# Performance work log

Hardware: AMD Instinct MI355X
Metric: run time of the kernel (lower is better)

Reference implementation:

```python
import jax, jax.numpy as jnp
import numpy as np

B, N, DIM = 4, 2048, 128
K = 32            # num_nearest_neighbors
FF = 4            # fourier_features
M_DIM = 16
EDGE_IN = FF * 2 + DIM * 2 + 1  # 265


def setup_inputs() -> dict:
    key = jax.random.key(0)
    ks = jax.random.split(key, 16)
    std = 0.001  # init_eps normal init for Linear weights
    p = {
        "feats": jax.random.normal(ks[0], (B, N, DIM), jnp.float32),
        "coors": jax.random.normal(ks[1], (B, N, 3), jnp.float32),
        # edge_mlp: Linear(265, 530) -> SiLU -> Linear(530, 16) -> SiLU
        "eW1": jax.random.normal(ks[2], (EDGE_IN, EDGE_IN * 2), jnp.float32) * std,
        "eb1": jax.random.normal(ks[3], (EDGE_IN * 2,), jnp.float32) * std,
        "eW2": jax.random.normal(ks[4], (EDGE_IN * 2, M_DIM), jnp.float32) * std,
        "eb2": jax.random.normal(ks[5], (M_DIM,), jnp.float32) * std,
        # coors_mlp: Linear(16, 64) -> SiLU -> Linear(64, 1)
        "cW1": jax.random.normal(ks[6], (M_DIM, M_DIM * 4), jnp.float32) * std,
        "cb1": jax.random.normal(ks[7], (M_DIM * 4,), jnp.float32) * std,
        "cW2": jax.random.normal(ks[8], (M_DIM * 4, 1), jnp.float32) * std,
        "cb2": jax.random.normal(ks[9], (1,), jnp.float32) * std,
        # node_mlp: Linear(144, 256) -> SiLU -> Linear(256, 128)
        "nW1": jax.random.normal(ks[10], (DIM + M_DIM, DIM * 2), jnp.float32) * std,
        "nb1": jax.random.normal(ks[11], (DIM * 2,), jnp.float32) * std,
        "nW2": jax.random.normal(ks[12], (DIM * 2, DIM), jnp.float32) * std,
        "nb2": jax.random.normal(ks[13], (DIM,), jnp.float32) * std,
    }
    return p


def _egnn_fwd(feats, coors, eW1, eb1, eW2, eb2, cW1, cb1, cW2, cb2, nW1, nb1, nW2, nb2):
    # all-pairs squared distances: [b, n, n]
    rel_coors_full = coors[:, :, None, :] - coors[:, None, :, :]
    rel_dist = jnp.sum(rel_coors_full * rel_coors_full, axis=-1)

    # top-k nearest (smallest distance) -> indices [b, n, k]
    _, idx = jax.lax.top_k(-rel_dist, K)

    # gather neighbor coords / feats per batch: [b, n, k, *]
    coors_j = jax.vmap(lambda x, i: x[i])(coors, idx)
    feats_j = jax.vmap(lambda x, i: x[i])(feats, idx)
    rel_coors = coors[:, :, None, :] - coors_j                     # b n k 3
    d = jnp.take_along_axis(rel_dist, idx, axis=2)[..., None]       # b n k 1

    # fourier encode distances: [b, n, k, 2*FF + 1]
    scales = 2.0 ** jnp.arange(FF, dtype=feats.dtype)               # [FF]
    xs = d[..., None] / scales                                      # b n k 1 FF
    enc = jnp.concatenate([jnp.sin(xs), jnp.cos(xs), d[..., None]], axis=-1)
    enc = enc[..., 0, :]                                            # b n k (2FF+1)

    feats_i = jnp.broadcast_to(feats[:, :, None, :], feats_j.shape)
    edge_input = jnp.concatenate([feats_i, feats_j, enc], axis=-1)  # b n k 265

    # edge MLP -> messages m_ij [b, n, k, m_dim]
    h = jax.nn.silu(edge_input @ eW1 + eb1)
    m_ij = jax.nn.silu(h @ eW2 + eb2)

    # coors MLP -> per-edge coordinate weights [b, n, k]
    cw = (jax.nn.silu(m_ij @ cW1 + cb1) @ cW2 + cb2)[..., 0]
    coors_out = jnp.einsum('bij,bijc->bic', cw, rel_coors) + coors

    # node update: sum-pool messages, concat with feats, MLP + residual
    m_i = jnp.sum(m_ij, axis=-2)                                    # b n m_dim
    node_in = jnp.concatenate([feats, m_i], axis=-1)
    node_out = jax.nn.silu(node_in @ nW1 + nb1) @ nW2 + nb2 + feats
    return node_out, coors_out


def reference(feats, coors, eW1, eb1, eW2, eb2, cW1, cb1, cW2, cb2, nW1, nb1, nW2, nb2):
    return _egnn_fwd(feats, coors, eW1, eb1, eW2, eb2, cW1, cb1, cW2, cb2, nW1, nb1, nW2, nb2)
```

## Files before the change

### kernel.cpp

```cpp
#include <hip/hip_runtime.h>
#include <hip/hip_bf16.h>
#include <math.h>

#define Bb 4
#define Nn 2048
#define DIMd 128
#define Kk 32
#define H1 530
#define PW2 530
#define MD 16
#define NDH 256
#define NDI 144
#define TOPK_BLKS (Bb*Nn/4)
#define PMAT_BLKS (Bb*Nn/32)

typedef float f32x2 __attribute__((ext_vector_type(2)));
typedef float f32x4 __attribute__((ext_vector_type(4)));
typedef short s16x8 __attribute__((ext_vector_type(8)));

__device__ __forceinline__ unsigned short f2bf(float f){
    union { float f; unsigned u; } v; v.f = f;
    unsigned r = v.u + 0x7FFFu + ((v.u >> 16) & 1u);
    return (unsigned short)(r >> 16);
}
__device__ __forceinline__ float silu_f(float x){
    float e = __builtin_amdgcn_exp2f(x * -1.442695041f);
    return x * __builtin_amdgcn_rcpf(1.0f + e);
}
__device__ __forceinline__ f32x2 silu2(f32x2 x){
    float e0 = __builtin_amdgcn_exp2f(x[0] * -1.442695041f);
    float e1 = __builtin_amdgcn_exp2f(x[1] * -1.442695041f);
    f32x2 r;
    r[0] = x[0] * __builtin_amdgcn_rcpf(1.0f + e0);
    r[1] = x[1] * __builtin_amdgcn_rcpf(1.0f + e1);
    return r;
}
__device__ __forceinline__ unsigned cvt_pk_bf16(float a, float b){
    unsigned r;
    asm("v_cvt_pk_bf16_f32 %0, %1, %2" : "=v"(r) : "v"(a), "v"(b));
    return r;
}

__global__ __launch_bounds__(256) void fragw_kernel(const float* __restrict__ eW1,
        const float* __restrict__ eW2,
        unsigned short* __restrict__ W1F, unsigned short* __restrict__ WPF,
        unsigned short* __restrict__ W2F2){
    int i0 = blockIdx.x * 256 + threadIdx.x;
    int stride = gridDim.x * 256;
    for (int i = i0; i < 34*5*512; i += stride){
        int j = i & 7, lane = (i >> 3) & 63, t = i >> 9;
        int ks = t % 5, nt = t / 5;
        int cg = nt*16 + (lane & 15);
        int k = ks*32 + ((lane >> 4) << 3) + j;
        float v = 0.f;
        if (cg < H1){
            if (k < 128) v = eW1[(size_t)(128+k)*H1 + cg];
            else if (k < 137) v = eW1[(size_t)(256+(k-128))*H1 + cg];
        }
        W1F[i] = f2bf(v);
    }
    for (int i = i0; i < 34*4*512; i += stride){
        int j = i & 7, lane = (i >> 3) & 63, t = i >> 9;
        int ks = t & 3, nt = t >> 2;
        int cg = nt*16 + (lane & 15);
        int k = ks*32 + ((lane >> 4) << 3) + j;
        float v = (cg < H1) ? eW1[(size_t)k*H1 + cg] : 0.f;
        WPF[i] = f2bf(v);
    }
    for (int i = i0; i < 34*512; i += stride){
        int j = i & 7, lane = (i >> 3) & 63, nt = i >> 9;
        int kl = ((lane >> 4) << 3) + j;
        int col = lane & 15;
        int row = nt*16 + kl;
        float v = (kl < 16 && row < H1) ? eW2[(size_t)row*MD + col] : 0.f;
        W2F2[i] = f2bf(v);
    }
}

__global__ __launch_bounds__(256) void prep_kernel(const float* __restrict__ coors,
        const float* __restrict__ feats,
        const unsigned short* __restrict__ WPF, const float* __restrict__ eb1,
        int* __restrict__ idx_ws, float* __restrict__ dv_ws, float* __restrict__ P){
    int bid = blockIdx.x;
    int tid = threadIdx.x;
    if (bid < TOPK_BLKS){
        int w = tid >> 6, lane = tid & 63;
        int node = bid * 4 + w;
        int b = node >> 11;
        const float* cbp = coors + (size_t)b * Nn * 3;
        float cx = coors[node*3+0], cy = coors[node*3+1], cz = coors[node*3+2];
        float d[32];
        #pragma unroll
        for (int t = 0; t < 32; t++){
            int j = t*64 + lane;
            float dx = cx - cbp[j*3+0], dy = cy - cbp[j*3+1], dz = cz - cbp[j*3+2];
            d[t] = dx*dx + dy*dy + dz*dz;
        }
        float md = d[0]; int mj = lane;
        #pragma unroll
        for (int t = 1; t < 32; t++){
            int jt = t*64 + lane;
            if (d[t] < md){ md = d[t]; mj = jt; }
        }
        for (int r = 0; r < Kk; r++){
            float bd = md; int bj = mj;
            #pragma unroll
            for (int off = 32; off; off >>= 1){
                float d2 = __shfl_xor(bd, off); int j2 = __shfl_xor(bj, off);
                if (d2 < bd || (d2 == bd && j2 < bj)){ bd = d2; bj = j2; }
            }
            if (lane == 0){
                idx_ws[node*Kk + r] = bj;
                dv_ws[node*Kk + r] = bd;
            }
            if (mj == bj){
                md = 3.4e38f; mj = 0x7fffffff;
                #pragma unroll
                for (int t = 0; t < 32; t++){
                    int jt = t*64 + lane;
                    if (jt == bj) d[t] = 3.4e38f;
                    if (d[t] < md){ md = d[t]; mj = jt; }
                }
            }
        }
    } else {
        int wid = tid >> 6, lane = tid & 63;
        int node0 = (bid - TOPK_BLKS) * 32;
        int kg = (lane >> 4) * 8;
        s16x8 af[2][4];
        #pragma unroll
        for (int m = 0; m < 2; m++){
            const float* fr = feats + (size_t)(node0 + m*16 + (lane & 15)) * DIMd;
            #pragma unroll
            for (int ks = 0; ks < 4; ks++){
                f32x4 lo = *(const f32x4*)(fr + ks*32 + kg);
                f32x4 hi = *(const f32x4*)(fr + ks*32 + kg + 4);
                union { s16x8 v; unsigned u[4]; } pk;
                pk.u[0] = cvt_pk_bf16(lo[0], lo[1]); pk.u[1] = cvt_pk_bf16(lo[2], lo[3]);
                pk.u[2] = cvt_pk_bf16(hi[0], hi[1]); pk.u[3] = cvt_pk_bf16(hi[2], hi[3]);
                af[m][ks] = pk.v;
            }
        }
        const s16x8* WPFv = (const s16x8*)WPF;
        for (int nt = wid; nt < 34; nt += 4){
            f32x4 acc0 = {0,0,0,0}, acc1 = {0,0,0,0};
            #pragma unroll
            for (int ks = 0; ks < 4; ks++){
                s16x8 bb = WPFv[(nt*4 + ks)*64 + lane];
                acc0 = __builtin_amdgcn_mfma_f32_16x16x32_bf16(af[0][ks], bb, acc0, 0, 0, 0);
                acc1 = __builtin_amdgcn_mfma_f32_16x16x32_bf16(af[1][ks], bb, acc1, 0, 0, 0);
            }
            int cg = nt*16 + (lane & 15);
            if (cg < H1){
                float b = eb1[cg];
                int r0 = (lane >> 4) * 4;
                #pragma unroll
                for (int r = 0; r < 4; r++){
                    P[(size_t)(node0 + r0 + r)*PW2 + cg]      = acc0[r] + b;
                    P[(size_t)(node0 + 16 + r0 + r)*PW2 + cg] = acc1[r] + b;
                }
            }
        }
    }
}

__global__ __launch_bounds__(256, 4) void edge_kernel(const float* __restrict__ coors,
        const float* __restrict__ feats, const float* __restrict__ eb2,
        const float* __restrict__ cW1, const float* __restrict__ cb1,
        const float* __restrict__ cW2, const float* __restrict__ cb2,
        const float* __restrict__ P, const unsigned short* __restrict__ W1F,
        const unsigned short* __restrict__ W2F2,
        const int* __restrict__ idx_ws, const float* __restrict__ dv_ws,
        float* __restrict__ mi_ws, float* __restrict__ coors_out){
    __shared__ float Pi_lds[544];
    __shared__ __align__(16) unsigned short aenc[Kk][32];
    __shared__ int js[Kk];
    __shared__ float rels[Kk][3];
    __shared__ float m_red[4][Kk][MD+1];
    __shared__ float cacc[4][3];

    int node = blockIdx.x; int tid = threadIdx.x;
    int b = node >> 11;
    int wid = tid >> 6, lane = tid & 63;

    const float* Pn = P + (size_t)node*PW2;
    Pi_lds[tid]       = Pn[tid];
    { int c = tid + 256; Pi_lds[c] = (c < PW2) ? Pn[c] : 0.f; }
    if (tid < 32){ int c = 512 + tid; Pi_lds[c] = (c < PW2) ? Pn[c] : 0.f; }
    if (tid < Kk){
        int j = idx_ws[node*Kk + tid];
        float dv = dv_ws[node*Kk + tid];
        js[tid] = j;
        unsigned short e[9];
        e[0] = f2bf(sinf(dv));        e[1] = f2bf(sinf(dv*0.5f));
        e[2] = f2bf(sinf(dv*0.25f));  e[3] = f2bf(sinf(dv*0.125f));
        e[4] = f2bf(cosf(dv));        e[5] = f2bf(cosf(dv*0.5f));
        e[6] = f2bf(cosf(dv*0.25f));  e[7] = f2bf(cosf(dv*0.125f));
        e[8] = f2bf(dv);
        #pragma unroll
        for (int q = 0; q < 9; q++) aenc[tid][q] = e[q];
        #pragma unroll
        for (int q = 9; q < 32; q++) aenc[tid][q] = 0;
        int jg = (b << 11) + j;
        rels[tid][0] = coors[node*3+0] - coors[jg*3+0];
        rels[tid][1] = coors[node*3+1] - coors[jg*3+1];
        rels[tid][2] = coors[node*3+2] - coors[jg*3+2];
    }
    __syncthreads();

    int kg = (lane >> 4) * 8;
    int grp = lane >> 4, n16 = lane & 15;
    s16x8 af[2][5];
    #pragma unroll
    for (int m = 0; m < 2; m++){
        int row = m*16 + n16;
        int jgl = (b << 11) + js[row];
        const float* fr = feats + (size_t)jgl * DIMd;
        #pragma unroll
        for (int ks = 0; ks < 4; ks++){
            f32x4 lo = *(const f32x4*)(fr + ks*32 + kg);
            f32x4 hi = *(const f32x4*)(fr + ks*32 + kg + 4);
            union { s16x8 v; unsigned u[4]; } pk;
            pk.u[0] = cvt_pk_bf16(lo[0], lo[1]); pk.u[1] = cvt_pk_bf16(lo[2], lo[3]);
            pk.u[2] = cvt_pk_bf16(hi[0], hi[1]); pk.u[3] = cvt_pk_bf16(hi[2], hi[3]);
            af[m][ks] = pk.v;
        }
        af[m][4] = *(const s16x8*)(&aenc[row][kg]);
    }

    int addr1 = ((((2*grp)    ) << 4) | n16) << 2;
    int addr2 = ((((2*grp) + 1) << 4) | n16) << 2;

    const s16x8* W1Fv  = (const s16x8*)W1F;
    const s16x8* W2F2v = (const s16x8*)W2F2;
    f32x4 macc0 = {0,0,0,0}, macc1 = {0,0,0,0};
    for (int nt = wid; nt < 34; nt += 4){
        f32x4 acc0 = {0,0,0,0}, acc1 = {0,0,0,0};
        #pragma unroll
        for (int ks = 0; ks < 5; ks++){
            s16x8 aw = W1Fv[(nt*5 + ks)*64 + lane];
            acc0 = __builtin_amdgcn_mfma_f32_16x16x32_bf16(aw, af[0][ks], acc0, 0, 0, 0);
            acc1 = __builtin_amdgcn_mfma_f32_16x16x32_bf16(aw, af[1][ks], acc1, 0, 0, 0);
        }
        s16x8 w2a = W2F2v[nt*64 + lane];
        int cgb = nt*16 + grp*4;
        float x0[4], x1[4];
        #pragma unroll
        for (int r = 0; r < 4; r++){
            int cg = cgb + r;
            bool valid = cg < H1;
            float pic = Pi_lds[cg];
            x0[r] = valid ? silu_f(acc0[r] + pic) : 0.f;
            x1[r] = valid ? silu_f(acc1[r] + pic) : 0.f;
        }
        unsigned p00 = cvt_pk_bf16(x0[0], x0[1]), p01 = cvt_pk_bf16(x0[2], x0[3]);
        unsigned p10 = cvt_pk_bf16(x1[0], x1[1]), p11 = cvt_pk_bf16(x1[2], x1[3]);
        union { s16x8 v; int u[4]; } b0, b1;
        b0.u[0] = __builtin_amdgcn_ds_bpermute(addr1, (int)p00);
        b0.u[1] = __builtin_amdgcn_ds_bpermute(addr1, (int)p01);
        b0.u[2] = __builtin_amdgcn_ds_bpermute(addr2, (int)p00);
        b0.u[3] = __builtin_amdgcn_ds_bpermute(addr2, (int)p01);
        b1.u[0] = __builtin_amdgcn_ds_bpermute(addr1, (int)p10);
        b1.u[1] = __builtin_amdgcn_ds_bpermute(addr1, (int)p11);
        b1.u[2] = __builtin_amdgcn_ds_bpermute(addr2, (int)p10);
        b1.u[3] = __builtin_amdgcn_ds_bpermute(addr2, (int)p11);
        macc0 = __builtin_amdgcn_mfma_f32_16x16x32_bf16(w2a, b0.v, macc0, 0, 0, 0);
        macc1 = __builtin_amdgcn_mfma_f32_16x16x32_bf16(w2a, b1.v, macc1, 0, 0, 0);
    }
    #pragma unroll
    for (int r = 0; r < 4; r++){
        m_red[wid][n16][grp*4 + r]      = macc0[r];
        m_red[wid][16 + n16][grp*4 + r] = macc1[r];
    }
    __syncthreads();
    #pragma unroll
    for (int t = tid; t < Kk*MD; t += 256){
        int n = t >> 4, f = t & 15;
        float s = m_red[0][n][f] + m_red[1][n][f] + m_red[2][n][f] + m_red[3][n][f];
        m_red[0][n][f] = silu_f(s + eb2[f]);
    }
    __syncthreads();
    if (tid < MD){
        float s = 0.f;
        #pragma unroll
        for (int n = 0; n < Kk; n++) s += m_red[0][n][tid];
        mi_ws[node*MD + tid] = s;
    }
    float vx = 0.f, vy = 0.f, vz = 0.f;
    int u4 = n16 * 4;
    f32x4 cb14 = *(const f32x4*)(cb1 + u4);
    f32x4 c24  = *(const f32x4*)(cW2 + u4);
    #pragma unroll
    for (int q = 0; q < 2; q++){
        int eid = wid*8 + grp*2 + q;
        f32x4 acc4 = cb14;
        #pragma unroll
        for (int f = 0; f < MD; f++){
            float mv = m_red[0][eid][f];
            f32x4 w4 = *(const f32x4*)(cW1 + f*64 + u4);
            acc4 += (f32x4){mv,mv,mv,mv} * w4;
        }
        float p = silu_f(acc4[0])*c24[0] + silu_f(acc4[1])*c24[1]
                + silu_f(acc4[2])*c24[2] + silu_f(acc4[3])*c24[3];
        #pragma unroll
        for (int off = 1; off < 16; off <<= 1) p += __shfl_xor(p, off);
        float cw = p + cb2[0];
        if (n16 == 0){
            vx += cw * rels[eid][0];
            vy += cw * rels[eid][1];
            vz += cw * rels[eid][2];
        }
    }
    vx += __shfl_xor(vx, 16); vx += __shfl_xor(vx, 32);
    vy += __shfl_xor(vy, 16); vy += __shfl_xor(vy, 32);
    vz += __shfl_xor(vz, 16); vz += __shfl_xor(vz, 32);
    if (lane == 0){ cacc[wid][0] = vx; cacc[wid][1] = vy; cacc[wid][2] = vz; }
    __syncthreads();
    if (tid == 0){
        coors_out[node*3+0] = cacc[0][0]+cacc[1][0]+cacc[2][0]+cacc[3][0] + coors[node*3+0];
        coors_out[node*3+1] = cacc[0][1]+cacc[1][1]+cacc[2][1]+cacc[3][1] + coors[node*3+1];
        coors_out[node*3+2] = cacc[0][2]+cacc[1][2]+cacc[2][2]+cacc[3][2] + coors[node*3+2];
    }
}

__global__ __launch_bounds__(256) void node_kernel(const float* __restrict__ feats,
        const float* __restrict__ mi_ws,
        const float* __restrict__ nW1, const float* __restrict__ nb1,
        const float* __restrict__ nW2, const float* __restrict__ nb2,
        float* __restrict__ out){
    __shared__ float insT[NDI][12];
    __shared__ float hsdT[NDH][12];
    int tid = threadIdx.x;
    int node0 = blockIdx.x * 8;
    for (int t = tid; t < 8*DIMd; t += 256){
        int m = t >> 7, k = t & 127;
        insT[k][m] = feats[(size_t)node0*DIMd + t];
    }
    if (tid < 8*MD) insT[DIMd + (tid & 15)][tid >> 4] = mi_ws[node0*MD + tid];
    __syncthreads();
    float bias = nb1[tid];
    f32x2 acc[4];
    #pragma unroll
    for (int p = 0; p < 4; p++) acc[p] = (f32x2){bias, bias};
    for (int k = 0; k < NDI; k++){
        float wv = nW1[(size_t)k*NDH + tid];
        f32x2 w2 = {wv, wv};
        acc[0] += *(const f32x2*)&insT[k][0] * w2;
        acc[1] += *(const f32x2*)&insT[k][2] * w2;
        acc[2] += *(const f32x2*)&insT[k][4] * w2;
        acc[3] += *(const f32x2*)&insT[k][6] * w2;
    }
    #pragma unroll
    for (int p = 0; p < 4; p++) *(f32x2*)&hsdT[tid][2*p] = silu2(acc[p]);
    __syncthreads();
    int c = tid & 127, half = tid >> 7;
    float b2 = nb2[c];
    f32x2 a0 = {b2, b2}, a1 = {b2, b2};
    for (int k = 0; k < NDH; k++){
        float wv = nW2[(size_t)k*DIMd + c];
        f32x2 w2 = {wv, wv};
        a0 += *(const f32x2*)&hsdT[k][half*4]     * w2;
        a1 += *(const f32x2*)&hsdT[k][half*4 + 2] * w2;
    }
    #pragma unroll
    for (int q = 0; q < 4; q++){
        int m = half*4 + q;
        float v = (q < 2) ? a0[q & 1] : a1[q & 1];
        out[(size_t)(node0+m)*DIMd + c] = v + feats[(size_t)(node0+m)*DIMd + c];
    }
}

extern "C" void kernel_launch(void* const* d_in, const int* in_sizes, int n_in,
                              void* d_out, int out_size, void* d_ws, size_t ws_size,
                              hipStream_t stream){
    const float* feats = (const float*)d_in[0];
    const float* coors = (const float*)d_in[1];
    const float* eW1 = (const float*)d_in[2];
    const float* eb1 = (const float*)d_in[3];
    const float* eW2 = (const float*)d_in[4];
    const float* eb2 = (const float*)d_in[5];
    const float* cW1 = (const float*)d_in[6];
    const float* cb1 = (const float*)d_in[7];
    const float* cW2 = (const float*)d_in[8];
    const float* cb2 = (const float*)d_in[9];
    const float* nW1 = (const float*)d_in[10];
    const float* nb1 = (const float*)d_in[11];
    const float* nW2 = (const float*)d_in[12];
    const float* nb2 = (const float*)d_in[13];
    float* out = (float*)d_out;
    float* coors_out = out + (size_t)Bb*Nn*DIMd;

    char* ws = (char*)d_ws;
    size_t off = 0;
    int*   idx_ws = (int*)(ws + off);   off += (1u<<20);
    float* dv_ws  = (float*)(ws + off); off += (1u<<20);
    float* Pd     = (float*)(ws + off); off += 17367040u;
    float* mi_ws  = (float*)(ws + off); off += 524288u;
    unsigned short* W1F  = (unsigned short*)(ws + off); off += 174080u;
    unsigned short* WPF  = (unsigned short*)(ws + off); off += 139264u;
    unsigned short* W2F2 = (unsigned short*)(ws + off); off += 34816u;

    fragw_kernel<<<256, 256, 0, stream>>>(eW1, eW2, W1F, WPF, W2F2);
    prep_kernel<<<TOPK_BLKS + PMAT_BLKS, 256, 0, stream>>>(coors, feats, WPF, eb1,
                                                           idx_ws, dv_ws, Pd);
    edge_kernel<<<Bb*Nn, 256, 0, stream>>>(coors, feats, eb2, cW1, cb1, cW2, cb2,
                                           Pd, W1F, W2F2, idx_ws, dv_ws, mi_ws, coors_out);
    node_kernel<<<Bb*Nn/8, 256, 0, stream>>>(feats, mi_ws, nW1, nb1, nW2, nb2, out);
}
```

Before: 321.1 us.

## Move coords MLP and message pooling from edge kernel into node kernel

The edge kernel now stops after producing per-edge messages and writes the full m_ij tensor to a new workspace. A new finish_kernel does the coors MLP per edge (one thread per edge), the message sum-pool and the node MLP, all in one place. This shrinks the edge kernel's register and LDS footprint so the launch bound can go from 4 to 6 waves, and it drops the bounds check in the SiLU loop. The cost is an extra 16 MB of global writes and reads for m_ij, and the padded columns now rely on zero weights and padded Pi_lds.

```diff
diff --git a/kernel.cpp b/kernel.cpp
--- a/kernel.cpp
+++ b/kernel.cpp
@@ -164,20 +164,16 @@
     }
 }
 
-__global__ __launch_bounds__(256, 4) void edge_kernel(const float* __restrict__ coors,
+__global__ __launch_bounds__(256, 6) void edge_kernel(
         const float* __restrict__ feats, const float* __restrict__ eb2,
-        const float* __restrict__ cW1, const float* __restrict__ cb1,
-        const float* __restrict__ cW2, const float* __restrict__ cb2,
         const float* __restrict__ P, const unsigned short* __restrict__ W1F,
         const unsigned short* __restrict__ W2F2,
         const int* __restrict__ idx_ws, const float* __restrict__ dv_ws,
-        float* __restrict__ mi_ws, float* __restrict__ coors_out){
+        float* __restrict__ m_ws){
     __shared__ float Pi_lds[544];
     __shared__ __align__(16) unsigned short aenc[Kk][32];
     __shared__ int js[Kk];
-    __shared__ float rels[Kk][3];
     __shared__ float m_red[4][Kk][MD+1];
-    __shared__ float cacc[4][3];
 
     int node = blockIdx.x; int tid = threadIdx.x;
     int b = node >> 11;
@@ -201,10 +197,6 @@
         for (int q = 0; q < 9; q++) aenc[tid][q] = e[q];
         #pragma unroll
         for (int q = 9; q < 32; q++) aenc[tid][q] = 0;
-        int jg = (b << 11) + j;
-        rels[tid][0] = coors[node*3+0] - coors[jg*3+0];
-        rels[tid][1] = coors[node*3+1] - coors[jg*3+1];
-        rels[tid][2] = coors[node*3+2] - coors[jg*3+2];
     }
     __syncthreads();
 
@@ -247,11 +239,9 @@
         float x0[4], x1[4];
         #pragma unroll
         for (int r = 0; r < 4; r++){
-            int cg = cgb + r;
-            bool valid = cg < H1;
-            float pic = Pi_lds[cg];
-            x0[r] = valid ? silu_f(acc0[r] + pic) : 0.f;
-            x1[r] = valid ? silu_f(acc1[r] + pic) : 0.f;
+            float pic = Pi_lds[cgb + r];
+            x0[r] = silu_f(acc0[r] + pic);
+            x1[r] = silu_f(acc1[r] + pic);
         }
         unsigned p00 = cvt_pk_bf16(x0[0], x0[1]), p01 = cvt_pk_bf16(x0[2], x0[3]);
         unsigned p10 = cvt_pk_bf16(x1[0], x1[1]), p11 = cvt_pk_bf16(x1[2], x1[3]);
@@ -277,71 +267,76 @@
     for (int t = tid; t < Kk*MD; t += 256){
         int n = t >> 4, f = t & 15;
         float s = m_red[0][n][f] + m_red[1][n][f] + m_red[2][n][f] + m_red[3][n][f];
-        m_red[0][n][f] = silu_f(s + eb2[f]);
-    }
-    __syncthreads();
-    if (tid < MD){
-        float s = 0.f;
-        #pragma unroll
-        for (int n = 0; n < Kk; n++) s += m_red[0][n][tid];
-        mi_ws[node*MD + tid] = s;
-    }
-    float vx = 0.f, vy = 0.f, vz = 0.f;
-    int u4 = n16 * 4;
-    f32x4 cb14 = *(const f32x4*)(cb1 + u4);
-    f32x4 c24  = *(const f32x4*)(cW2 + u4);
-    #pragma unroll
-    for (int q = 0; q < 2; q++){
-        int eid = wid*8 + grp*2 + q;
-        f32x4 acc4 = cb14;
-        #pragma unroll
-        for (int f = 0; f < MD; f++){
-            float mv = m_red[0][eid][f];
-            f32x4 w4 = *(const f32x4*)(cW1 + f*64 + u4);
-            acc4 += (f32x4){mv,mv,mv,mv} * w4;
-        }
-        float p = silu_f(acc4[0])*c24[0] + silu_f(acc4[1])*c24[1]
-                + silu_f(acc4[2])*c24[2] + silu_f(acc4[3])*c24[3];
-        #pragma unroll
-        for (int off = 1; off < 16; off <<= 1) p += __shfl_xor(p, off);
-        float cw = p + cb2[0];
-        if (n16 == 0){
-            vx += cw * rels[eid][0];
-            vy += cw * rels[eid][1];
-            vz += cw * rels[eid][2];
-        }
-    }
-    vx += __shfl_xor(vx, 16); vx += __shfl_xor(vx, 32);
-    vy += __shfl_xor(vy, 16); vy += __shfl_xor(vy, 32);
-    vz += __shfl_xor(vz, 16); vz += __shfl_xor(vz, 32);
-    if (lane == 0){ cacc[wid][0] = vx; cacc[wid][1] = vy; cacc[wid][2] = vz; }
-    __syncthreads();
-    if (tid == 0){
-        coors_out[node*3+0] = cacc[0][0]+cacc[1][0]+cacc[2][0]+cacc[3][0] + coors[node*3+0];
-        coors_out[node*3+1] = cacc[0][1]+cacc[1][1]+cacc[2][1]+cacc[3][1] + coors[node*3+1];
-        coors_out[node*3+2] = cacc[0][2]+cacc[1][2]+cacc[2][2]+cacc[3][2] + coors[node*3+2];
-    }
-}
-
-__global__ __launch_bounds__(256) void node_kernel(const float* __restrict__ feats,
-        const float* __restrict__ mi_ws,
+        m_ws[(size_t)node*(Kk*MD) + t] = silu_f(s + eb2[f]);
+    }
+}
+
+__global__ __launch_bounds__(256) void finish_kernel(const float* __restrict__ feats,
+        const float* __restrict__ coors,
+        const float* __restrict__ m_ws, const int* __restrict__ idx_ws,
+        const float* __restrict__ cW1, const float* __restrict__ cb1,
+        const float* __restrict__ cW2, const float* __restrict__ cb2,
         const float* __restrict__ nW1, const float* __restrict__ nb1,
         const float* __restrict__ nW2, const float* __restrict__ nb2,
-        float* __restrict__ out){
+        float* __restrict__ out, float* __restrict__ coors_out){
+    __shared__ float msh[8][Kk][MD+1];
     __shared__ float insT[NDI][12];
     __shared__ float hsdT[NDH][12];
     int tid = threadIdx.x;
     int node0 = blockIdx.x * 8;
-    for (int t = tid; t < 8*DIMd; t += 256){
-        int m = t >> 7, k = t & 127;
-        insT[k][m] = feats[(size_t)node0*DIMd + t];
-    }
-    if (tid < 8*MD) insT[DIMd + (tid & 15)][tid >> 4] = mi_ws[node0*MD + tid];
+    const float* mp = m_ws + (size_t)node0*(Kk*MD);
+    for (int t = tid; t < 8*Kk*MD; t += 256)
+        msh[t >> 9][(t >> 4) & 31][t & 15] = mp[t];
+    for (int t = tid; t < 8*DIMd; t += 256)
+        insT[t & 127][t >> 7] = feats[(size_t)node0*DIMd + t];
+    int nl = tid >> 5, n = tid & 31;
+    int node = node0 + nl;
+    int b = node >> 11;
+    int j = idx_ws[node*Kk + n];
+    int jg = (b << 11) + j;
+    float rx = coors[node*3+0] - coors[jg*3+0];
+    float ry = coors[node*3+1] - coors[jg*3+1];
+    float rz = coors[node*3+2] - coors[jg*3+2];
+    __syncthreads();
+    if (tid < 128){
+        int m = tid >> 4, f = tid & 15;
+        float s = 0.f;
+        #pragma unroll
+        for (int q = 0; q < Kk; q++) s += msh[m][q][f];
+        insT[DIMd + f][m] = s;
+    }
+    float mv[MD];
+    #pragma unroll
+    for (int f = 0; f < MD; f++) mv[f] = msh[nl][n][f];
+    float p = 0.f;
+    #pragma unroll 4
+    for (int ug = 0; ug < 16; ug++){
+        f32x4 a4 = *(const f32x4*)(cb1 + ug*4);
+        #pragma unroll
+        for (int f = 0; f < MD; f++){
+            f32x4 w4 = *(const f32x4*)(cW1 + f*64 + ug*4);
+            a4 += (f32x4){mv[f],mv[f],mv[f],mv[f]} * w4;
+        }
+        f32x4 c4 = *(const f32x4*)(cW2 + ug*4);
+        p += silu_f(a4[0])*c4[0] + silu_f(a4[1])*c4[1]
+           + silu_f(a4[2])*c4[2] + silu_f(a4[3])*c4[3];
+    }
+    float cw = p + cb2[0];
+    float vx = cw*rx, vy = cw*ry, vz = cw*rz;
+    #pragma unroll
+    for (int off = 1; off < 32; off <<= 1){
+        vx += __shfl_xor(vx, off); vy += __shfl_xor(vy, off); vz += __shfl_xor(vz, off);
+    }
+    if (n == 0){
+        coors_out[node*3+0] = vx + coors[node*3+0];
+        coors_out[node*3+1] = vy + coors[node*3+1];
+        coors_out[node*3+2] = vz + coors[node*3+2];
+    }
     __syncthreads();
     float bias = nb1[tid];
     f32x2 acc[4];
     #pragma unroll
-    for (int p = 0; p < 4; p++) acc[p] = (f32x2){bias, bias};
+    for (int q = 0; q < 4; q++) acc[q] = (f32x2){bias, bias};
     for (int k = 0; k < NDI; k++){
         float wv = nW1[(size_t)k*NDH + tid];
         f32x2 w2 = {wv, wv};
@@ -351,7 +346,7 @@
         acc[3] += *(const f32x2*)&insT[k][6] * w2;
     }
     #pragma unroll
-    for (int p = 0; p < 4; p++) *(f32x2*)&hsdT[tid][2*p] = silu2(acc[p]);
+    for (int q = 0; q < 4; q++) *(f32x2*)&hsdT[tid][2*q] = silu2(acc[q]);
     __syncthreads();
     int c = tid & 127, half = tid >> 7;
     float b2 = nb2[c];
@@ -395,7 +390,7 @@
     int*   idx_ws = (int*)(ws + off);   off += (1u<<20);
     float* dv_ws  = (float*)(ws + off); off += (1u<<20);
     float* Pd     = (float*)(ws + off); off += 17367040u;
-    float* mi_ws  = (float*)(ws + off); off += 524288u;
+    float* m_ws   = (float*)(ws + off); off += 16777216u;
     unsigned short* W1F  = (unsigned short*)(ws + off); off += 174080u;
     unsigned short* WPF  = (unsigned short*)(ws + off); off += 139264u;
     unsigned short* W2F2 = (unsigned short*)(ws + off); off += 34816u;
@@ -403,7 +398,9 @@
     fragw_kernel<<<256, 256, 0, stream>>>(eW1, eW2, W1F, WPF, W2F2);
     prep_kernel<<<TOPK_BLKS + PMAT_BLKS, 256, 0, stream>>>(coors, feats, WPF, eb1,
                                                            idx_ws, dv_ws, Pd);
-    edge_kernel<<<Bb*Nn, 256, 0, stream>>>(coors, feats, eb2, cW1, cb1, cW2, cb2,
-                                           Pd, W1F, W2F2, idx_ws, dv_ws, mi_ws, coors_out);
-    node_kernel<<<Bb*Nn/8, 256, 0, stream>>>(feats, mi_ws, nW1, nb1, nW2, nb2, out);
-}
+    edge_kernel<<<Bb*Nn, 256, 0, stream>>>(feats, eb2, Pd, W1F, W2F2,
+                                           idx_ws, dv_ws, m_ws);
+    finish_kernel<<<Bb*Nn/8, 256, 0, stream>>>(feats, coors, m_ws, idx_ws,
+                                               cW1, cb1, cW2, cb2,
+                                               nW1, nb1, nW2, nb2, out, coors_out);
+}
```

Result: faster. 297.3 us (-7.4%).
